# Kernel optimization log

Measured on AMD Instinct MI355X. Metric: run time of the kernel, lower is better.

## Reference

```python
import jax, jax.numpy as jnp
import numpy as np

D_MODEL = 512
NUM_HEADS = 8
HEAD_DIM = 64  # D_MODEL // NUM_HEADS


def setup_inputs() -> dict:
    key = jax.random.key(0)
    kq, kk, kv, kw, kb = jax.random.split(key, 5)
    B, S = 2, 2048
    query = jax.random.normal(kq, (B, S, D_MODEL), dtype=jnp.float32)
    key_t = jax.random.normal(kk, (B, S, D_MODEL), dtype=jnp.float32)
    value = jax.random.normal(kv, (B, S, D_MODEL), dtype=jnp.float32)
    # shared projection (nn.Linear(d_models, d_models)) applied to q, k, v
    scale = 1.0 / np.sqrt(D_MODEL)
    W = jax.random.uniform(kw, (D_MODEL, D_MODEL), dtype=jnp.float32, minval=-scale, maxval=scale)
    b = jax.random.uniform(kb, (D_MODEL,), dtype=jnp.float32, minval=-scale, maxval=scale)
    return {"query": query, "key": key_t, "value": value, "W": W, "b": b}


def reference(query, key, value, W, b):
    B, S, _ = query.shape
    H, Dh = NUM_HEADS, HEAD_DIM

    def proj(x):  # nn.Linear + ReLU, shared across q/k/v
        return jax.nn.relu(jnp.einsum('bsd,ed->bse', x, W) + b)

    # [B, S, d] -> [B, H, S, Dh]
    split = lambda x: proj(x).reshape(B, S, H, Dh).transpose(0, 2, 1, 3)
    Q, K, V = split(query), split(key), split(value)

    scores = jnp.einsum('bhqd,bhkd->bhqk', Q, K) / jnp.sqrt(jnp.float32(Dh))
    causal_mask = jnp.triu(jnp.ones((S, S), dtype=bool), k=1)  # True above diagonal
    scores = jnp.where(causal_mask, -jnp.inf, scores)
    attn = jax.nn.softmax(scores, axis=-1)
    out = jnp.einsum('bhqk,bhkd->bhqd', attn, V)  # [B, H, S, Dh]

    # faithful to original: transpose(0,1) swaps batch and heads, then view
    final = jnp.swapaxes(out, 0, 1).reshape(B, -1, D_MODEL)  # [B, S, d_model]
    return final
```

## Files before the change

### kernel.cpp

```cpp
#include <hip/hip_runtime.h>
#include <hip/hip_bf16.h>
#include <cstdint>
#include <cstddef>

typedef __bf16 bf16_t;
typedef bf16_t bf16x8 __attribute__((ext_vector_type(8)));
typedef float f32x4 __attribute__((ext_vector_type(4)));
typedef float f32x16 __attribute__((ext_vector_type(16)));
typedef unsigned short u16;
typedef u16 u16x8 __attribute__((ext_vector_type(8)));

#define S_LEN 2048
#define NB 2
#define NH 8
#define DHD 64
#define DM 512

static __device__ __forceinline__ u16 bfbits(float f) {
  union { __bf16 h; u16 u; } c; c.h = (__bf16)f; return c.u;
}
static __device__ __forceinline__ float bits2f(u16 b) {
  union { u16 u; __bf16 h; } c; c.u = b; return (float)c.h;
}
static __device__ __forceinline__ uint32_t pkbf(float a, float b) {
  union { __bf16 h[2]; uint32_t u; } c;
  c.h[0] = (__bf16)a; c.h[1] = (__bf16)b;
  return c.u;
}
static __device__ __forceinline__ void gload16(const void* g, void* l) {
  __builtin_amdgcn_global_load_lds(
      (const __attribute__((address_space(1))) uint32_t*)g,
      (__attribute__((address_space(3))) uint32_t*)l, 16, 0, 0);
}

static __device__ __forceinline__ int slot_of(int bh, int t32, int chunk) {
  int qb = t32 >> 2;
  int nc = (2 * (qb + 1) + 9) / 10;
  int off;
  if (qb < 10) off = (qb - 5) * 8;
  else if (qb < 15) off = 40 + (qb - 10) * 12;
  else off = 100;
  return bh * 116 + off + (t32 & 3) * nc + chunk;
}

__launch_bounds__(256, 2)
__global__ void proj_kernel(const float* __restrict__ Xq, const float* __restrict__ Xk,
                            const float* __restrict__ Xv, const float* __restrict__ W,
                            const float* __restrict__ bias,
                            u16* __restrict__ Qw, u16* __restrict__ Kw,
                            u16* __restrict__ Vt64) {
  __shared__ __align__(16) float BUF[2][8192];
  const int bid = blockIdx.x;
  const int xcd = bid & 7;
  const int u = bid >> 3;
  const int n0 = (u & 3) * 128;
  const int mIdx = u >> 2;
  const int mg = (xcd * 12 + mIdx) * 128;
  const int z = mg >> 12;
  const int m_in = mg & 4095;
  const int b = m_in >> 11;
  const int s0m = m_in & (S_LEN - 1);
  const int h0 = n0 >> 6;
  const float* __restrict__ X = (z == 0) ? Xq : ((z == 1) ? Xk : Xv);
  X += (size_t)m_in * DM;

  const int t = threadIdx.x;
  const int lane = t & 63;
  const int wid = t >> 6;
  const int wr = wid >> 1, wc = wid & 1;
  const int fr = lane & 15, fg = lane >> 4;

  f32x4 acc[4][4] = {};

  const int lrow = lane >> 3;
  const int lblk = lane & 7;

  auto stage = [&](int bf, int k0) {
    #pragma unroll
    for (int i = 0; i < 4; ++i) {
      int c = wid * 4 + i;
      int r = c * 8 + lrow;
      gload16(X + (size_t)r * DM + k0 + ((lblk ^ (r & 7)) << 2), &BUF[bf][c * 256]);
    }
    #pragma unroll
    for (int i = 0; i < 4; ++i) {
      int c = wid * 4 + i;
      int r = c * 8 + lrow;
      gload16(W + (size_t)(n0 + r) * DM + k0 + ((lblk ^ (r & 7)) << 2),
              &BUF[bf][4096 + c * 256]);
    }
  };

  stage(0, 0);
  int cb = 0;
  for (int i = 0; i < 16; ++i) {
    __syncthreads();
    if (i < 15) stage(cb ^ 1, (i + 1) * 32);
    const float* Ac = BUF[cb];
    bf16x8 af[4], bfr[4];
    #pragma unroll
    for (int m2 = 0; m2 < 4; ++m2) {
      int r = wr*64 + m2*16 + fr;
      f32x4 lo = *(const f32x4*)&Ac[r*32 + (((2*fg)     ^ (r & 7)) << 2)];
      f32x4 hi = *(const f32x4*)&Ac[r*32 + (((2*fg + 1) ^ (r & 7)) << 2)];
      union { u16x8 s; bf16x8 v; } f;
      f.s[0]=bfbits(lo[0]); f.s[1]=bfbits(lo[1]); f.s[2]=bfbits(lo[2]); f.s[3]=bfbits(lo[3]);
      f.s[4]=bfbits(hi[0]); f.s[5]=bfbits(hi[1]); f.s[6]=bfbits(hi[2]); f.s[7]=bfbits(hi[3]);
      af[m2] = f.v;
    }
    #pragma unroll
    for (int ni = 0; ni < 4; ++ni) {
      int r = wc*64 + ni*16 + fr;
      f32x4 lo = *(const f32x4*)&Ac[4096 + r*32 + (((2*fg)     ^ (r & 7)) << 2)];
      f32x4 hi = *(const f32x4*)&Ac[4096 + r*32 + (((2*fg + 1) ^ (r & 7)) << 2)];
      union { u16x8 s; bf16x8 v; } f;
      f.s[0]=bfbits(lo[0]); f.s[1]=bfbits(lo[1]); f.s[2]=bfbits(lo[2]); f.s[3]=bfbits(lo[3]);
      f.s[4]=bfbits(hi[0]); f.s[5]=bfbits(hi[1]); f.s[6]=bfbits(hi[2]); f.s[7]=bfbits(hi[3]);
      bfr[ni] = f.v;
    }
    __builtin_amdgcn_s_setprio(1);
    #pragma unroll
    for (int m2 = 0; m2 < 4; ++m2)
      #pragma unroll
      for (int ni = 0; ni < 4; ++ni)
        acc[m2][ni] = __builtin_amdgcn_mfma_f32_16x16x32_bf16(af[m2], bfr[ni], acc[m2][ni], 0, 0, 0);
    __builtin_amdgcn_s_setprio(0);
    cb ^= 1;
  }
  __syncthreads();

  const float QSCALE = 0.125f * 1.44269504089f;
  u16* epi = (u16*)&BUF[0][0];

  if (z == 2) {
    #pragma unroll
    for (int m2 = 0; m2 < 4; ++m2) {
      #pragma unroll
      for (int ni = 0; ni < 4; ++ni) {
        int e = wc*64 + ni*16 + fr;
        int m = wr*64 + m2*16 + fg*4;
        float bv = bias[n0 + e];
        float v0 = fmaxf(acc[m2][ni][0] + bv, 0.f);
        float v1 = fmaxf(acc[m2][ni][1] + bv, 0.f);
        float v2 = fmaxf(acc[m2][ni][2] + bv, 0.f);
        float v3 = fmaxf(acc[m2][ni][3] + bv, 0.f);
        uint2 w; w.x = pkbf(v0, v1); w.y = pkbf(v2, v3);
        *(uint2*)&epi[e*136 + m] = w;
      }
    }
    __syncthreads();
    const int e2 = t >> 1, mc = (t & 1) * 64;
    const int h = h0 + (e2 >> 6), d = e2 & 63;
    const int sb = (s0m >> 6) + (mc >> 6);
    u16* dst = Vt64 + (((size_t)(b * NH + h) * 32 + sb) * 64 + d) * 64;
    #pragma unroll
    for (int i = 0; i < 8; ++i)
      *(uint4*)(dst + i*8) = *(const uint4*)&epi[e2*136 + mc + i*8];
  } else {
    #pragma unroll
    for (int m2 = 0; m2 < 4; ++m2) {
      #pragma unroll
      for (int ni = 0; ni < 4; ++ni) {
        int e = wc*64 + ni*16 + fr;
        float bv = bias[n0 + e];
        #pragma unroll
        for (int r = 0; r < 4; ++r) {
          float v = acc[m2][ni][r] + bv;
          if (z == 0) v *= QSCALE;
          v = fmaxf(v, 0.f);
          epi[(wr*64 + m2*16 + fg*4 + r)*136 + e] = bfbits(v);
        }
      }
    }
    __syncthreads();
    const int mrow = t >> 1, hf = t & 1;
    u16* dst = ((z == 0) ? Qw : Kw) +
               (((size_t)(b * NH + h0 + hf)) * S_LEN + s0m + mrow) * DHD;
    #pragma unroll
    for (int i = 0; i < 8; ++i)
      *(uint4*)(dst + i*8) = *(const uint4*)&epi[mrow*136 + hf*64 + i*8];
  }
}

static __device__ const uint8_t QBT[34] = {4,5,6,7,8,9,9,10,10,11,11,12,12,13,13,14,14,14,15,15,15,
                                           3,8,13, 2,7,12, 1,6,11, 0,5,10,15};
static __device__ const uint8_t CKT[34] = {0,0,0,0,0,0,1,0,1,0,1,0,1,0,1,0,1,2,0,1,2,
                                           0,1,2, 0,1,2, 0,1,2, 0,1,2,3};

__launch_bounds__(256, 3)
__global__ void attn_kernel(const u16* __restrict__ Qw, const u16* __restrict__ Kw,
                            const u16* __restrict__ Vt64, u16* __restrict__ Opart,
                            float* __restrict__ lbuf, float* __restrict__ out) {
  __shared__ u16 KLDS[2][4096];
  __shared__ u16 VLDS[2][4096];
  const int t = threadIdx.x;
  const int lane = t & 63;
  const int wid = t >> 6;
  const int lam = lane & 31;
  const int hi = lane >> 5;
  const int h8 = hi << 3, h4 = hi << 2;
  const int bid = blockIdx.x;
  const int bh = bid & 15;
  const int u = bid >> 4;
  const int qb = QBT[u], chunk = CKT[u];
  const int steps_total = (qb + 1) * 2;
  const int sc0 = chunk * 10;
  const int sc1e = sc0 + 10;
  const int sc1 = (sc1e < steps_total) ? sc1e : steps_total;
  const int t32 = qb * 4 + wid;
  const int q0 = qb * 128 + wid * 32;

  const u16* __restrict__ Qh = Qw + (size_t)bh * S_LEN * DHD;
  const u16* __restrict__ Kh = Kw + (size_t)bh * S_LEN * DHD;
  const u16* __restrict__ V64 = Vt64 + (size_t)bh * 32 * 64 * 64;

  bf16x8 qf[4];
  #pragma unroll
  for (int c = 0; c < 4; ++c)
    qf[c] = *(const bf16x8*)(Qh + (size_t)(q0 + lam) * DHD + c*16 + h8);

  const int lrow = lane >> 3;
  const int lblk = lane & 7;
  auto stage = [&](int bf, int s) {
    #pragma unroll
    for (int i = 0; i < 2; ++i) {
      int c = wid * 2 + i;
      int r = c * 8 + lrow;
      int sw = (lblk ^ (r & 7)) << 3;
      gload16(Kh + (size_t)(s * 64 + r) * 64 + sw, &KLDS[bf][c * 512]);
      gload16(V64 + ((size_t)s * 64 + r) * 64 + sw, &VLDS[bf][c * 512]);
    }
  };

  f32x16 o0 = {}, o1 = {};
  float lsum = 0.f;

  auto softpack = [&](const f32x16& sc, bool msk, bf16x8& pb0v, bf16x8& pb1v) {
    float p[16];
    #pragma unroll
    for (int r = 0; r < 16; ++r) {
      float ev = __builtin_amdgcn_exp2f(sc[r]);
      int kc = (r & 3) + ((r >> 2) << 3) + h4;
      if (msk && kc > lam) ev = 0.f;
      p[r] = ev;
      lsum += ev;
    }
    uint32_t X0 = pkbf(p[0], p[1]),  X1 = pkbf(p[2], p[3]);
    uint32_t X2 = pkbf(p[4], p[5]),  X3 = pkbf(p[6], p[7]);
    uint32_t X4 = pkbf(p[8], p[9]),  X5 = pkbf(p[10], p[11]);
    uint32_t X6 = pkbf(p[12], p[13]), X7 = pkbf(p[14], p[15]);
    asm("v_permlane32_swap_b32 %0, %1" : "+v"(X0), "+v"(X2));
    asm("v_permlane32_swap_b32 %0, %1" : "+v"(X1), "+v"(X3));
    asm("v_permlane32_swap_b32 %0, %1" : "+v"(X4), "+v"(X6));
    asm("v_permlane32_swap_b32 %0, %1" : "+v"(X5), "+v"(X7));
    union U8 { uint32_t u[4]; bf16x8 v; };
    U8 a, bU;
    a.u[0] = X0; a.u[1] = X1; a.u[2] = X2; a.u[3] = X3;
    bU.u[0] = X4; bU.u[1] = X5; bU.u[2] = X6; bU.u[3] = X7;
    pb0v = a.v; pb1v = bU.v;
  };

  stage(0, sc0);
  int cb = 0;
  for (int s = sc0; s < sc1; ++s) {
    __syncthreads();
    if (s + 1 < sc1) stage(cb ^ 1, s + 1);
    const int d2 = t32 - 2 * s;
    bf16x8 a0, a1, b0v, b1v;
    f32x16 sA = {}, sB = {};
    if (d2 >= 0) {
      bf16x8 kA[4];
      #pragma unroll
      for (int c = 0; c < 4; ++c) {
        int r = lam, e = ((2*c + hi) ^ (r & 7)) * 8;
        kA[c] = *(const bf16x8*)&KLDS[cb][r*64 + e];
      }
      __builtin_amdgcn_s_setprio(1);
      #pragma unroll
      for (int c = 0; c < 4; ++c)
        sA = __builtin_amdgcn_mfma_f32_32x32x16_bf16(kA[c], qf[c], sA, 0, 0, 0);
      __builtin_amdgcn_s_setprio(0);
    }
    if (d2 >= 1) {
      bf16x8 kB[4];
      #pragma unroll
      for (int c = 0; c < 4; ++c) {
        int r = 32 + lam, e = ((2*c + hi) ^ (r & 7)) * 8;
        kB[c] = *(const bf16x8*)&KLDS[cb][r*64 + e];
      }
      __builtin_amdgcn_s_setprio(1);
      #pragma unroll
      for (int c = 0; c < 4; ++c)
        sB = __builtin_amdgcn_mfma_f32_32x32x16_bf16(kB[c], qf[c], sB, 0, 0, 0);
      __builtin_amdgcn_s_setprio(0);
    }
    if (d2 >= 0) softpack(sA, d2 == 0, a0, a1);
    if (d2 >= 1) softpack(sB, d2 == 1, b0v, b1v);
    if (d2 >= 0) {
      bf16x8 v0[2], v1[2];
      #pragma unroll
      for (int c2 = 0; c2 < 2; ++c2) {
        int r0 = lam,      e0 = ((2*c2 + hi) ^ (r0 & 7)) * 8;
        int r1 = 32 + lam, e1 = ((2*c2 + hi) ^ (r1 & 7)) * 8;
        v0[c2] = *(const bf16x8*)&VLDS[cb][r0*64 + e0];
        v1[c2] = *(const bf16x8*)&VLDS[cb][r1*64 + e1];
      }
      __builtin_amdgcn_s_setprio(1);
      o0 = __builtin_amdgcn_mfma_f32_32x32x16_bf16(v0[0], a0, o0, 0, 0, 0);
      o0 = __builtin_amdgcn_mfma_f32_32x32x16_bf16(v0[1], a1, o0, 0, 0, 0);
      o1 = __builtin_amdgcn_mfma_f32_32x32x16_bf16(v1[0], a0, o1, 0, 0, 0);
      o1 = __builtin_amdgcn_mfma_f32_32x32x16_bf16(v1[1], a1, o1, 0, 0, 0);
      __builtin_amdgcn_s_setprio(0);
    }
    if (d2 >= 1) {
      bf16x8 v0[2], v1[2];
      #pragma unroll
      for (int c2 = 0; c2 < 2; ++c2) {
        int r0 = lam,      e0 = ((4 + 2*c2 + hi) ^ (r0 & 7)) * 8;
        int r1 = 32 + lam, e1 = ((4 + 2*c2 + hi) ^ (r1 & 7)) * 8;
        v0[c2] = *(const bf16x8*)&VLDS[cb][r0*64 + e0];
        v1[c2] = *(const bf16x8*)&VLDS[cb][r1*64 + e1];
      }
      __builtin_amdgcn_s_setprio(1);
      o0 = __builtin_amdgcn_mfma_f32_32x32x16_bf16(v0[0], b0v, o0, 0, 0, 0);
      o0 = __builtin_amdgcn_mfma_f32_32x32x16_bf16(v0[1], b1v, o0, 0, 0, 0);
      o1 = __builtin_amdgcn_mfma_f32_32x32x16_bf16(v1[0], b0v, o1, 0, 0, 0);
      o1 = __builtin_amdgcn_mfma_f32_32x32x16_bf16(v1[1], b1v, o1, 0, 0, 0);
      __builtin_amdgcn_s_setprio(0);
    }
    cb ^= 1;
  }

  float l = lsum + __shfl_xor(lsum, 32);

  if (qb <= 4) {
    const int b = bh >> 3, hh = bh & 7;
    const float inv = 1.0f / l;
    float* orow = out + (((size_t)(hh * NB + b)) * S_LEN + (q0 + lam)) * DHD;
    #pragma unroll
    for (int r = 0; r < 16; ++r) {
      int d = (r & 3) + ((r >> 2) << 3) + h4;
      orow[d] = o0[r] * inv;
      orow[d + 32] = o1[r] * inv;
    }
  } else {
    const int slot = slot_of(bh, t32, chunk);
    uint32_t w[16] __attribute__((aligned(16)));
    #pragma unroll
    for (int m = 0; m < 8; ++m) {
      w[m]     = pkbf(o0[2*m], o0[2*m+1]);
      w[8 + m] = pkbf(o1[2*m], o1[2*m+1]);
    }
    u16* op = Opart + (size_t)slot * 2048 + (size_t)lane * 32;
    #pragma unroll
    for (int i = 0; i < 4; ++i)
      *(uint4*)(op + i*8) = *(const uint4*)&w[i*4];
    if (lane < 32) lbuf[slot * 32 + lane] = l;
  }
}

__launch_bounds__(256)
__global__ void reduce_kernel(const u16* __restrict__ Opart,
                              const float* __restrict__ lbuf,
                              float* __restrict__ out) {
  const int t = threadIdx.x;
  const int unit = blockIdx.x * 4 + (t >> 6);
  const int bh = unit & 15;
  const int ti = 20 + (unit >> 4);
  const int qb = ti >> 2;
  const int nc = (2 * (qb + 1) + 9) / 10;
  const int lane = t & 63;
  const int lam = lane & 31;
  const int h4 = (lane >> 5) << 2;
  const int slot0 = slot_of(bh, ti, 0);

  float O[32];
  #pragma unroll
  for (int i = 0; i < 32; ++i) O[i] = 0.f;
  float L = 0.f;

  for (int c = 0; c < nc; ++c) {
    const u16* op = Opart + (size_t)(slot0 + c) * 2048 + (size_t)lane * 32;
    L += lbuf[(slot0 + c) * 32 + lam];
    #pragma unroll
    for (int i = 0; i < 4; ++i) {
      uint4 v = *(const uint4*)(op + i*8);
      uint32_t a[4] = {v.x, v.y, v.z, v.w};
      #pragma unroll
      for (int jj = 0; jj < 4; ++jj) {
        O[i*8 + 2*jj]     += bits2f((u16)(a[jj] & 0xFFFFu));
        O[i*8 + 2*jj + 1] += bits2f((u16)(a[jj] >> 16));
      }
    }
  }

  const int b = bh >> 3, hh = bh & 7;
  const float inv = 1.0f / L;
  float* orow = out + (((size_t)(hh * NB + b)) * S_LEN + (ti*32 + lam)) * DHD;
  #pragma unroll
  for (int r = 0; r < 16; ++r) {
    int d = (r & 3) + ((r >> 2) << 3) + h4;
    orow[d] = O[r] * inv;
    orow[d + 32] = O[16 + r] * inv;
  }
}

extern "C" void kernel_launch(void* const* d_in, const int* in_sizes, int n_in,
                              void* d_out, int out_size, void* d_ws, size_t ws_size,
                              hipStream_t stream) {
  const float* q = (const float*)d_in[0];
  const float* k = (const float*)d_in[1];
  const float* v = (const float*)d_in[2];
  const float* W = (const float*)d_in[3];
  const float* b = (const float*)d_in[4];

  const size_t elems = (size_t)NB * NH * S_LEN * DHD;
  u16* Qw = (u16*)d_ws;
  u16* Kw = Qw + elems;
  u16* Vt64 = Kw + elems;
  u16* Opart = Vt64 + elems;
  float* lbuf = (float*)(Opart + (size_t)1856 * 2048);

  proj_kernel<<<dim3(384), dim3(256), 0, stream>>>(q, k, v, W, b, Qw, Kw, Vt64);

  attn_kernel<<<dim3(544), dim3(256), 0, stream>>>(Qw, Kw, Vt64, Opart, lbuf, (float*)d_out);

  reduce_kernel<<<dim3(176), dim3(256), 0, stream>>>(Opart, lbuf, (float*)d_out);
}
```

Baseline: 50.51 us.

## Keep full W head slice in LDS as bf16, stream X directly from global

The projection kernel changes its tile from 128x128 with K-staged double buffering to 256 rows by one 64-column head. The block first converts its entire 64x512 W slice to bf16 in swizzled LDS once. It then streams X fragments straight from global memory into MFMA operands, with no LDS staging or per-step barriers. This drops the sync and LDS traffic for the A operand, at the cost of uncoalesced direct global loads of X, exposed latency in the main loop, and a larger LDS footprint that may lower occupancy.

```diff
diff --git a/kernel.cpp b/kernel.cpp
--- a/kernel.cpp
+++ b/kernel.cpp
@@ -49,136 +49,126 @@
                             const float* __restrict__ bias,
                             u16* __restrict__ Qw, u16* __restrict__ Kw,
                             u16* __restrict__ Vt64) {
-  __shared__ __align__(16) float BUF[2][8192];
+  __shared__ __align__(16) u16 POOL[32768];
   const int bid = blockIdx.x;
   const int xcd = bid & 7;
   const int u = bid >> 3;
-  const int n0 = (u & 3) * 128;
-  const int mIdx = u >> 2;
-  const int mg = (xcd * 12 + mIdx) * 128;
+  const int nq = u & 7;
+  const int mgrp = xcd * 6 + (u >> 3);
+  const int mg = mgrp * 256;
   const int z = mg >> 12;
   const int m_in = mg & 4095;
   const int b = m_in >> 11;
   const int s0m = m_in & (S_LEN - 1);
-  const int h0 = n0 >> 6;
-  const float* __restrict__ X = (z == 0) ? Xq : ((z == 1) ? Xk : Xv);
-  X += (size_t)m_in * DM;
+  const size_t bhh = (size_t)(b * NH + nq);
 
   const int t = threadIdx.x;
   const int lane = t & 63;
   const int wid = t >> 6;
-  const int wr = wid >> 1, wc = wid & 1;
   const int fr = lane & 15, fg = lane >> 4;
 
+  {
+    const float* Wq = W + (size_t)(nq * 64) * DM;
+    const int wrow = t >> 2;
+    const int cbase = (t & 3) << 4;
+    #pragma unroll 4
+    for (int j = 0; j < 16; ++j) {
+      int c = cbase + j;
+      const float* p = Wq + (size_t)wrow * DM + c * 8;
+      float4 lo = *(const float4*)p, hi = *(const float4*)(p + 4);
+      u16x8 rr;
+      rr[0]=bfbits(lo.x); rr[1]=bfbits(lo.y); rr[2]=bfbits(lo.z); rr[3]=bfbits(lo.w);
+      rr[4]=bfbits(hi.x); rr[5]=bfbits(hi.y); rr[6]=bfbits(hi.z); rr[7]=bfbits(hi.w);
+      *(u16x8*)&POOL[wrow * 512 + ((c ^ (wrow & 15)) << 3)] = rr;
+    }
+  }
+  __syncthreads();
+
+  const float* __restrict__ Xz = ((z == 0) ? Xq : (z == 1) ? Xk : Xv) + (size_t)m_in * DM;
+  const int w64 = wid * 64;
+  const float* pA[4];
+  #pragma unroll
+  for (int mi = 0; mi < 4; ++mi)
+    pA[mi] = Xz + (size_t)(w64 + mi * 16 + fr) * DM + fg * 8;
+
   f32x4 acc[4][4] = {};
 
-  const int lrow = lane >> 3;
-  const int lblk = lane & 7;
-
-  auto stage = [&](int bf, int k0) {
-    #pragma unroll
-    for (int i = 0; i < 4; ++i) {
-      int c = wid * 4 + i;
-      int r = c * 8 + lrow;
-      gload16(X + (size_t)r * DM + k0 + ((lblk ^ (r & 7)) << 2), &BUF[bf][c * 256]);
-    }
-    #pragma unroll
-    for (int i = 0; i < 4; ++i) {
-      int c = wid * 4 + i;
-      int r = c * 8 + lrow;
-      gload16(W + (size_t)(n0 + r) * DM + k0 + ((lblk ^ (r & 7)) << 2),
-              &BUF[bf][4096 + c * 256]);
-    }
-  };
-
-  stage(0, 0);
-  int cb = 0;
-  for (int i = 0; i < 16; ++i) {
+  #pragma unroll
+  for (int kk = 0; kk < 16; ++kk) {
+    const int k0 = kk * 32;
+    bf16x8 af[4];
+    #pragma unroll
+    for (int mi = 0; mi < 4; ++mi) {
+      float4 lo = *(const float4*)(pA[mi] + k0);
+      float4 hi = *(const float4*)(pA[mi] + k0 + 4);
+      union { u16x8 s; bf16x8 v; } f;
+      f.s[0]=bfbits(lo.x); f.s[1]=bfbits(lo.y); f.s[2]=bfbits(lo.z); f.s[3]=bfbits(lo.w);
+      f.s[4]=bfbits(hi.x); f.s[5]=bfbits(hi.y); f.s[6]=bfbits(hi.z); f.s[7]=bfbits(hi.w);
+      af[mi] = f.v;
+    }
+    bf16x8 bfr[4];
+    #pragma unroll
+    for (int ni = 0; ni < 4; ++ni) {
+      int r = ni * 16 + fr;
+      int c = kk * 4 + fg;
+      bfr[ni] = *(const bf16x8*)&POOL[r * 512 + ((c ^ (r & 15)) << 3)];
+    }
+    __builtin_amdgcn_s_setprio(1);
+    #pragma unroll
+    for (int mi = 0; mi < 4; ++mi)
+      #pragma unroll
+      for (int ni = 0; ni < 4; ++ni)
+        acc[mi][ni] = __builtin_amdgcn_mfma_f32_16x16x32_bf16(af[mi], bfr[ni], acc[mi][ni], 0, 0, 0);
+    __builtin_amdgcn_s_setprio(0);
+  }
+
+  const float QSCALE = 0.125f * 1.44269504089f;
+  __syncthreads();
+
+  if (z == 2) {
+    #pragma unroll
+    for (int mi = 0; mi < 4; ++mi) {
+      #pragma unroll
+      for (int ni = 0; ni < 4; ++ni) {
+        int e = ni * 16 + fr;
+        int m = w64 + mi * 16 + fg * 4;
+        float bv = bias[nq * 64 + e];
+        float v0 = fmaxf(acc[mi][ni][0] + bv, 0.f);
+        float v1 = fmaxf(acc[mi][ni][1] + bv, 0.f);
+        float v2 = fmaxf(acc[mi][ni][2] + bv, 0.f);
+        float v3 = fmaxf(acc[mi][ni][3] + bv, 0.f);
+        uint2 w; w.x = pkbf(v0, v1); w.y = pkbf(v2, v3);
+        *(uint2*)&POOL[e * 264 + m] = w;
+      }
+    }
     __syncthreads();
-    if (i < 15) stage(cb ^ 1, (i + 1) * 32);
-    const float* Ac = BUF[cb];
-    bf16x8 af[4], bfr[4];
-    #pragma unroll
-    for (int m2 = 0; m2 < 4; ++m2) {
-      int r = wr*64 + m2*16 + fr;
-      f32x4 lo = *(const f32x4*)&Ac[r*32 + (((2*fg)     ^ (r & 7)) << 2)];
-      f32x4 hi = *(const f32x4*)&Ac[r*32 + (((2*fg + 1) ^ (r & 7)) << 2)];
-      union { u16x8 s; bf16x8 v; } f;
-      f.s[0]=bfbits(lo[0]); f.s[1]=bfbits(lo[1]); f.s[2]=bfbits(lo[2]); f.s[3]=bfbits(lo[3]);
-      f.s[4]=bfbits(hi[0]); f.s[5]=bfbits(hi[1]); f.s[6]=bfbits(hi[2]); f.s[7]=bfbits(hi[3]);
-      af[m2] = f.v;
-    }
-    #pragma unroll
-    for (int ni = 0; ni < 4; ++ni) {
-      int r = wc*64 + ni*16 + fr;
-      f32x4 lo = *(const f32x4*)&Ac[4096 + r*32 + (((2*fg)     ^ (r & 7)) << 2)];
-      f32x4 hi = *(const f32x4*)&Ac[4096 + r*32 + (((2*fg + 1) ^ (r & 7)) << 2)];
-      union { u16x8 s; bf16x8 v; } f;
-      f.s[0]=bfbits(lo[0]); f.s[1]=bfbits(lo[1]); f.s[2]=bfbits(lo[2]); f.s[3]=bfbits(lo[3]);
-      f.s[4]=bfbits(hi[0]); f.s[5]=bfbits(hi[1]); f.s[6]=bfbits(hi[2]); f.s[7]=bfbits(hi[3]);
-      bfr[ni] = f.v;
-    }
-    __builtin_amdgcn_s_setprio(1);
-    #pragma unroll
-    for (int m2 = 0; m2 < 4; ++m2)
-      #pragma unroll
-      for (int ni = 0; ni < 4; ++ni)
-        acc[m2][ni] = __builtin_amdgcn_mfma_f32_16x16x32_bf16(af[m2], bfr[ni], acc[m2][ni], 0, 0, 0);
-    __builtin_amdgcn_s_setprio(0);
-    cb ^= 1;
-  }
-  __syncthreads();
-
-  const float QSCALE = 0.125f * 1.44269504089f;
-  u16* epi = (u16*)&BUF[0][0];
-
-  if (z == 2) {
-    #pragma unroll
-    for (int m2 = 0; m2 < 4; ++m2) {
+    const int e = t >> 2, seg = t & 3;
+    const int sb = (s0m >> 6) + seg;
+    u16* dst = Vt64 + (((size_t)bhh * 32 + sb) * 64 + e) * 64;
+    #pragma unroll
+    for (int i = 0; i < 8; ++i)
+      *(uint4*)(dst + i * 8) = *(const uint4*)&POOL[e * 264 + seg * 64 + i * 8];
+  } else {
+    #pragma unroll
+    for (int mi = 0; mi < 4; ++mi) {
       #pragma unroll
       for (int ni = 0; ni < 4; ++ni) {
-        int e = wc*64 + ni*16 + fr;
-        int m = wr*64 + m2*16 + fg*4;
-        float bv = bias[n0 + e];
-        float v0 = fmaxf(acc[m2][ni][0] + bv, 0.f);
-        float v1 = fmaxf(acc[m2][ni][1] + bv, 0.f);
-        float v2 = fmaxf(acc[m2][ni][2] + bv, 0.f);
-        float v3 = fmaxf(acc[m2][ni][3] + bv, 0.f);
-        uint2 w; w.x = pkbf(v0, v1); w.y = pkbf(v2, v3);
-        *(uint2*)&epi[e*136 + m] = w;
-      }
-    }
-    __syncthreads();
-    const int e2 = t >> 1, mc = (t & 1) * 64;
-    const int h = h0 + (e2 >> 6), d = e2 & 63;
-    const int sb = (s0m >> 6) + (mc >> 6);
-    u16* dst = Vt64 + (((size_t)(b * NH + h) * 32 + sb) * 64 + d) * 64;
-    #pragma unroll
-    for (int i = 0; i < 8; ++i)
-      *(uint4*)(dst + i*8) = *(const uint4*)&epi[e2*136 + mc + i*8];
-  } else {
-    #pragma unroll
-    for (int m2 = 0; m2 < 4; ++m2) {
-      #pragma unroll
-      for (int ni = 0; ni < 4; ++ni) {
-        int e = wc*64 + ni*16 + fr;
-        float bv = bias[n0 + e];
+        int e = ni * 16 + fr;
+        float bv = bias[nq * 64 + e];
         #pragma unroll
         for (int r = 0; r < 4; ++r) {
-          float v = acc[m2][ni][r] + bv;
+          float v = acc[mi][ni][r] + bv;
           if (z == 0) v *= QSCALE;
           v = fmaxf(v, 0.f);
-          epi[(wr*64 + m2*16 + fg*4 + r)*136 + e] = bfbits(v);
+          POOL[(w64 + mi * 16 + fg * 4 + r) * 72 + e] = bfbits(v);
         }
       }
     }
     __syncthreads();
-    const int mrow = t >> 1, hf = t & 1;
-    u16* dst = ((z == 0) ? Qw : Kw) +
-               (((size_t)(b * NH + h0 + hf)) * S_LEN + s0m + mrow) * DHD;
+    u16* dst = ((z == 0) ? Qw : Kw) + (bhh * S_LEN + s0m + t) * DHD;
     #pragma unroll
     for (int i = 0; i < 8; ++i)
-      *(uint4*)(dst + i*8) = *(const uint4*)&epi[mrow*136 + hf*64 + i*8];
+      *(uint4*)(dst + i * 8) = *(const uint4*)&POOL[t * 72 + i * 8];
   }
 }
 
```

Measured after the change: 73.16 us. 44.8% more time.
